# Kernel optimization log

Measured on AMD Instinct MI355X. Metric: run time of the kernel, lower is better.

The kernel has to match this reference:

```python
import jax, jax.numpy as jnp
import numpy as np

D_MODEL, D_QKV, N_HEADS = 1024, 64, 16


def setup_inputs() -> dict:
    key = jax.random.key(0)
    k_x, k_qkv, k_out = jax.random.split(key, 3)
    X = jax.random.normal(k_x, (2, 2048, D_MODEL), dtype=jnp.float32)
    # nn.Linear(d_model, 3*d_qkv*n_heads, bias=False): store as (in, out) for X @ W
    W_qkv = jax.random.normal(k_qkv, (D_MODEL, 3 * D_QKV * N_HEADS), dtype=jnp.float32) * (D_MODEL ** -0.5)
    W_out = jax.random.normal(k_out, (D_QKV * N_HEADS, D_MODEL), dtype=jnp.float32) * ((D_QKV * N_HEADS) ** -0.5)
    return {"X": X, "W_qkv": W_qkv, "W_out": W_out}


def reference(X, W_qkv, W_out):
    b, s, _ = X.shape
    h, d = N_HEADS, D_QKV
    scale = d ** 0.5
    qkv = X @ W_qkv                          # [b, s, 3*h*d]
    # Faithful to torch: view(b, s, h, d, 3).unbind(-1) -> interleaved q/k/v layout
    qkv = qkv.reshape(b, s, h, d, 3)
    q, k, v = qkv[..., 0], qkv[..., 1], qkv[..., 2]   # each [b, s, h, d]
    scores = jnp.einsum("bqhd,bkhd->bhqk", q, k) / scale
    weights = jax.nn.softmax(scores, axis=-1)          # [b, h, s, s]
    attn = jnp.einsum("bhqk,bkhd->bqhd", weights, v)   # [b, s, h, d]
    return attn.reshape(b, s, h * d) @ W_out           # [b, s, d_model]
```

## Files before the change

### kernel.cpp

```cpp
#include <hip/hip_runtime.h>
#include <hip/hip_bf16.h>
#include <math.h>

typedef __bf16 bf16;
typedef __bf16 bf16x2 __attribute__((ext_vector_type(2)));
typedef __bf16 bf16x4 __attribute__((ext_vector_type(4)));
typedef __bf16 bf16x8 __attribute__((ext_vector_type(8)));
typedef float f32x2 __attribute__((ext_vector_type(2)));
typedef float f32x4 __attribute__((ext_vector_type(4)));
typedef float f32x16 __attribute__((ext_vector_type(16)));
typedef int i32x2 __attribute__((ext_vector_type(2)));
typedef int i32x4 __attribute__((ext_vector_type(4)));

#define MFMA16(a, b, c) __builtin_amdgcn_mfma_f32_16x16x32_bf16(a, b, c, 0, 0, 0)
#define MFMA32(a, b, c) __builtin_amdgcn_mfma_f32_32x32x16_bf16(a, b, c, 0, 0, 0)

constexpr int D_MODEL = 1024;
constexpr int N_QKV   = 3072;
constexpr int BATCH   = 2;
constexpr int SEQ     = 2048;
constexpr int NH      = 16;
constexpr int DH      = 64;
constexpr int M_TOT   = BATCH * SEQ;

__device__ __forceinline__ void gl_lds16(const bf16* g, bf16* l) {
    __builtin_amdgcn_global_load_lds(
        (const __attribute__((address_space(1))) void*)g,
        (__attribute__((address_space(3))) void*)l, 16, 0, 0);
}

__device__ __forceinline__ void pl32swap(int& a, int& b) {
    i32x2 r = __builtin_amdgcn_permlane32_swap(a, b, false, false);
    a = r[0];
    b = r[1];
}

template <int N> __device__ __forceinline__ void waitv() {
    asm volatile("s_waitcnt vmcnt(%0)" :: "n"(N) : "memory");
}
__device__ __forceinline__ void waitlgkm0() {
    asm volatile("s_waitcnt lgkmcnt(0)" ::: "memory");
}

__device__ __forceinline__ void transpose_tile(
    const float* __restrict__ in, bf16* __restrict__ out,
    int K, int N, int n0, int k0, bf16 (*T)[72], bool permute)
{
    const int tid = threadIdx.x;
    const int r   = tid >> 2;
    const int c4  = (tid & 3) * 16;

    const float* src = in + (size_t)(k0 + r) * N + n0 + c4;
    f32x4 v0 = *(const f32x4*)(src + 0);
    f32x4 v1 = *(const f32x4*)(src + 4);
    f32x4 v2 = *(const f32x4*)(src + 8);
    f32x4 v3 = *(const f32x4*)(src + 12);
    #pragma unroll
    for (int j = 0; j < 4; j++) {
        T[c4 + j][r]      = (bf16)v0[j];
        T[c4 + 4 + j][r]  = (bf16)v1[j];
        T[c4 + 8 + j][r]  = (bf16)v2[j];
        T[c4 + 12 + j][r] = (bf16)v3[j];
    }
    __syncthreads();
    int rowg = n0 + r;
    if (permute) {
        const int which = rowg % 3;
        const int h     = rowg / 192;
        const int d     = (rowg % 192) / 3;
        rowg = which * 1024 + h * 64 + d;
    }
    bf16* dst = out + (size_t)rowg * K + k0 + c4;
    *(bf16x8*)(dst)     = *(const bf16x8*)&T[r][c4];
    *(bf16x8*)(dst + 8) = *(const bf16x8*)&T[r][c4 + 8];
}

__global__ __launch_bounds__(256) void prepass_kernel(
    const float* __restrict__ X, const float* __restrict__ Wqkv,
    const float* __restrict__ Wout,
    bf16* __restrict__ xb, bf16* __restrict__ wqkv_t, bf16* __restrict__ wout_t)
{
    __shared__ bf16 T[64][72];
    const int b = blockIdx.x;
    if (b < 2048) {
        const size_t i = ((size_t)b * 256 + threadIdx.x) * 8;
        f32x4 a0 = *(const f32x4*)(X + i);
        f32x4 a1 = *(const f32x4*)(X + i + 4);
        bf16x8 w;
        #pragma unroll
        for (int j = 0; j < 4; j++) { w[j] = (bf16)a0[j]; w[j + 4] = (bf16)a1[j]; }
        *(bf16x8*)(xb + i) = w;
    } else if (b < 2048 + 768) {
        const int idx = b - 2048;
        transpose_tile(Wqkv, wqkv_t, D_MODEL, N_QKV,
                       (idx % 48) * 64, (idx / 48) * 64, T, true);
    } else {
        const int idx = b - 2816;
        transpose_tile(Wout, wout_t, D_MODEL, D_MODEL,
                       (idx % 16) * 64, (idx / 16) * 64, T, false);
    }
}

__global__ __launch_bounds__(512, 2) void qkv_gemm_kernel(
    const bf16* __restrict__ Xb, const bf16* __restrict__ Wt,
    bf16* __restrict__ qb, bf16* __restrict__ kb, bf16* __restrict__ vb)
{
    __shared__ __align__(16) bf16 smem[65536];
    bf16* const sA = smem;
    bf16* const sB = smem + 32768;

    const int tid  = threadIdx.x;
    const int wave = tid >> 6;
    const int lane = tid & 63;
    const int quad = lane >> 4;
    const int l16  = lane & 15;
    const int wr   = wave >> 2;
    const int wc   = wave & 3;
    const int m0   = blockIdx.x * 256;
    const int n0   = blockIdx.y * 256;

    const int sr2  = tid >> 3;
    const int c8p  = (tid & 7) ^ (sr2 & 7);
    const int stR0 = (sr2 << 1) | (c8p >> 2);
    const int stC0 = (c8p & 3) << 3;

    const bf16* Asrc = Xb + (size_t)(m0 + stR0) * D_MODEL + stC0;
    const bf16* Bsrc = Wt + (size_t)(n0 + stR0) * D_MODEL + stC0;

#define STG(s, kbo)                                                          \
    do {                                                                     \
        gl_lds16(Asrc + (kbo),                 sA + (s) * 8192 + tid * 8);   \
        gl_lds16(Asrc + 128 * D_MODEL + (kbo), sA + (s) * 8192 + 4096 + tid * 8); \
        gl_lds16(Bsrc + (kbo),                 sB + (s) * 8192 + tid * 8);   \
        gl_lds16(Bsrc + 128 * D_MODEL + (kbo), sB + (s) * 8192 + 4096 + tid * 8); \
    } while (0)

    const int foff = ((l16 >> 1) << 6) +
                     (((((l16 & 1) << 2) | quad) ^ ((l16 >> 1) & 7)) << 3);

    f32x4 acc[8][4];
    #pragma unroll
    for (int a = 0; a < 8; a++)
        #pragma unroll
        for (int b = 0; b < 4; b++) acc[a][b] = {0.f, 0.f, 0.f, 0.f};

    bf16x8 afA[8], bfA[4], afB[8], bfB[4];

    STG(0, 0); STG(1, 32); STG(2, 64);
    waitv<4>();
    __builtin_amdgcn_s_barrier();
    {
        const bf16* A0 = sA + wr * 4096;
        const bf16* B0 = sB + wc * 2048;
        #pragma unroll
        for (int mi = 0; mi < 8; mi++)
            afA[mi] = *(const bf16x8*)&A0[mi * 512 + foff];
        #pragma unroll
        for (int ni = 0; ni < 4; ni++)
            bfA[ni] = *(const bf16x8*)&B0[ni * 512 + foff];
    }

    int p = 0;

#define PHASE(CA, CB, NA, NB, DOSTG, DONXT, WV)                              \
    {                                                                        \
        if (DOSTG) { const int kst = p + 3; STG((kst & 3), kst * 32); }      \
        const int sn = (p + 1) & 3;                                          \
        const bf16* An_ = sA + sn * 8192 + wr * 4096;                        \
        const bf16* Bn_ = sB + sn * 8192 + wc * 2048;                        \
        __builtin_amdgcn_s_setprio(1);                                       \
        _Pragma("unroll") for (int c = 0; c < 4; c++) {                      \
            _Pragma("unroll") for (int m2 = 0; m2 < 2; m2++)                 \
                _Pragma("unroll") for (int ni = 0; ni < 4; ni++)             \
                    acc[c * 2 + m2][ni] =                                    \
                        MFMA16(CA[c * 2 + m2], CB[ni], acc[c * 2 + m2][ni]); \
            if (DONXT) {                                                     \
                NA[c * 2]     = *(const bf16x8*)&An_[(c * 2) * 512 + foff];  \
                NA[c * 2 + 1] = *(const bf16x8*)&An_[(c * 2 + 1) * 512 + foff]; \
            }                                                                \
        }                                                                    \
        if (DONXT) {                                                         \
            _Pragma("unroll") for (int ni = 0; ni < 4; ni++)                 \
                NB[ni] = *(const bf16x8*)&Bn_[ni * 512 + foff];              \
        }                                                                    \
        __builtin_amdgcn_s_setprio(0);                                       \
        waitv<WV>();                                                         \
        __builtin_amdgcn_s_barrier();                                        \
        ++p;                                                                 \
    }

    for (int t = 0; t < 14; ++t) {
        PHASE(afA, bfA, afB, bfB, true, true, 4)
        PHASE(afB, bfB, afA, bfA, true, true, 4)
    }
    PHASE(afA, bfA, afB, bfB, true,  true,  4)
    PHASE(afB, bfB, afA, bfA, false, true,  0)
    PHASE(afA, bfA, afB, bfB, false, true,  0)
    PHASE(afB, bfB, afA, bfA, false, false, 0)

#undef PHASE
#undef STG

    const int bb     = m0 >> 11;
    const int s_base = m0 & (SEQ - 1);

    if (n0 < 2048) {
        bf16* dst0 = (n0 < 1024) ? qb : kb;
        const int h = ((n0 + wc * 64) >> 6) & 15;
        const size_t bh = (size_t)(bb * NH + h);
        #pragma unroll
        for (int mi = 0; mi < 8; mi++) {
            const int s0 = s_base + wr * 128 + mi * 16 + quad * 4;
            #pragma unroll
            for (int ni = 0; ni < 4; ni++) {
                const int d = ni * 16 + l16;
                #pragma unroll
                for (int i = 0; i < 4; i++)
                    dst0[(bh * SEQ + s0 + i) * DH + d] = (bf16)acc[mi][ni][i];
            }
        }
    } else {
        __syncthreads();
        bf16* T = smem;
        #pragma unroll
        for (int ni = 0; ni < 4; ni++) {
            const int nl = wc * 64 + ni * 16 + l16;
            #pragma unroll
            for (int mi = 0; mi < 8; mi++) {
                const int ml = wr * 128 + mi * 16 + quad * 4;
                bf16x4 pv;
                #pragma unroll
                for (int i = 0; i < 4; i++) pv[i] = (bf16)acc[mi][ni][i];
                const int c   = ml >> 3;
                const int swz = (c & 24) | ((c ^ nl) & 7);
                *(bf16x4*)&T[nl * 256 + swz * 8 + (ml & 7)] = pv;
            }
        }
        __syncthreads();
        const int hbase = (n0 - 2048) >> 6;
        #pragma unroll
        for (int it = 0; it < 8; it++) {
            const int nl = (tid >> 4) + it * 32;
            const int h  = hbase + (nl >> 6);
            const int d  = nl & 63;
            const size_t obase = ((size_t)(bb * NH + h) * DH + d) * SEQ + s_base;
            #pragma unroll
            for (int cc = 0; cc < 2; cc++) {
                const int c   = (tid & 15) + cc * 16;
                const int swz = (c & 24) | ((c ^ nl) & 7);
                bf16x8 vv = *(const bf16x8*)&T[nl * 256 + swz * 8];
                *(bf16x8*)(vb + obase + c * 8) = vv;
            }
        }
    }
}

__global__ __launch_bounds__(512, 4) void attn_kernel(
    const bf16* __restrict__ qb, const bf16* __restrict__ kb,
    const bf16* __restrict__ vb, bf16* __restrict__ ob)
{
    __shared__ __align__(16) bf16 smem[32768];

    const int tid  = threadIdx.x;
    const int wave = tid >> 6;
    const int grp  = wave >> 2;
    const int wq   = wave & 3;
    const int lane = tid & 63;
    const int l32  = lane & 31;
    const int hi   = lane >> 5;
    const int ltid = tid & 255;
    const int bh   = blockIdx.x;
    const int q0   = blockIdx.y * 128;
    const size_t base  = (size_t)bh * SEQ * DH;
    const int    kbase = grp * (SEQ / 2);

    bf16* const KsB = smem + grp * 2 * 4096;
    bf16* const VtB = smem + 16384 + grp * 2 * 4096;

    constexpr float QSCALE = 0.125f * 1.44269504f;

    bf16x8 qf[4];
    {
        const size_t qoff = base + (size_t)(q0 + wq * 32 + l32) * DH + hi * 8;
        #pragma unroll
        for (int kc = 0; kc < 4; kc++) {
            qf[kc] = *(const bf16x8*)(qb + qoff + kc * 16);
            #pragma unroll
            for (int j = 0; j < 8; j++)
                qf[kc][j] = (bf16)((float)qf[kc][j] * QSCALE);
        }
    }

    f32x16 o_acc[2];
    #pragma unroll
    for (int i = 0; i < 16; i++) { o_acc[0][i] = 0.f; o_acc[1][i] = 0.f; }
    float l_acc = 0.f;

    const int swz = (l32 & 7) ^ (l32 >> 3);

    const int so0 = ltid;
    const int so1 = 256 + ltid;
    const int sr0 = so0 >> 3, sc0 = ((so0 & 7) ^ (sr0 & 7) ^ ((sr0 >> 3) & 3)) * 8;
    const int sr1 = so1 >> 3, sc1 = ((so1 & 7) ^ (sr1 & 7) ^ ((sr1 >> 3) & 3)) * 8;

    #define STAGE(bufi, kk0)                                                   \
        do {                                                                   \
            gl_lds16(kb + base + (size_t)(kbase + (kk0) + sr0) * DH + sc0,     \
                     KsB + (bufi) * 4096 + so0 * 8);                           \
            gl_lds16(kb + base + (size_t)(kbase + (kk0) + sr1) * DH + sc1,     \
                     KsB + (bufi) * 4096 + so1 * 8);                           \
            gl_lds16(vb + base + (size_t)sr0 * SEQ + kbase + (kk0) + sc0,      \
                     VtB + (bufi) * 4096 + so0 * 8);                           \
            gl_lds16(vb + base + (size_t)sr1 * SEQ + kbase + (kk0) + sc1,      \
                     VtB + (bufi) * 4096 + so1 * 8);                           \
        } while (0)

    STAGE(0, 0);
    int buf = 0;

    for (int kt = 0; kt < SEQ / 128; ++kt) {
        __syncthreads();
        if (kt + 1 < SEQ / 128) STAGE(buf ^ 1, (kt + 1) * 64);

        const bf16* Kst = KsB + buf * 4096;
        const bf16* Vtt = VtB + buf * 4096;

        #pragma unroll
        for (int kblk = 0; kblk < 2; kblk++) {
            f32x16 sacc;
            #pragma unroll
            for (int i = 0; i < 16; i++) sacc[i] = 0.f;
            #pragma unroll
            for (int kc = 0; kc < 4; kc++) {
                const int cko = ((2 * kc + hi) ^ swz) * 8;
                bf16x8 kf = *(const bf16x8*)
                    &Kst[(kblk * 32 + l32) * 64 + cko];
                sacc = MFMA32(kf, qf[kc], sacc);
            }

            int w[8];
            #pragma unroll
            for (int c = 0; c < 8; c++) {
                const float e0 = __builtin_amdgcn_exp2f(sacc[2 * c]);
                const float e1 = __builtin_amdgcn_exp2f(sacc[2 * c + 1]);
                l_acc += e0;
                l_acc += e1;
                bf16x2 t; t[0] = (bf16)e0; t[1] = (bf16)e1;
                w[c] = __builtin_bit_cast(int, t);
            }
            #pragma unroll
            for (int cc = 0; cc < 2; cc++) {
                pl32swap(w[cc * 4 + 0], w[cc * 4 + 2]);
                pl32swap(w[cc * 4 + 1], w[cc * 4 + 3]);
                i32x4 fi = {w[cc * 4 + 0], w[cc * 4 + 1],
                            w[cc * 4 + 2], w[cc * 4 + 3]};
                bf16x8 pa = __builtin_bit_cast(bf16x8, fi);

                const int kc = kblk * 2 + cc;
                const int cko = ((2 * kc + hi) ^ swz) * 8;
                #pragma unroll
                for (int nb = 0; nb < 2; nb++) {
                    bf16x8 vf = *(const bf16x8*)
                        &Vtt[(nb * 32 + l32) * 64 + cko];
                    o_acc[nb] = MFMA32(pa, vf, o_acc[nb]);
                }
            }
        }
        buf ^= 1;
    }
    #undef STAGE

    const float l_q = l_acc + __shfl_xor(l_acc, 32);

    float* cO  = (float*)smem;
    float* cL1 = (float*)smem + 8192;
    float* cL2 = (float*)smem + 8320;

    __syncthreads();
    if (grp == 1) {
        #pragma unroll
        for (int nb = 0; nb < 2; nb++)
            #pragma unroll
            for (int c4 = 0; c4 < 4; c4++) {
                const int j = nb * 4 + c4;
                f32x4 v = { o_acc[nb][c4 * 4 + 0], o_acc[nb][c4 * 4 + 1],
                            o_acc[nb][c4 * 4 + 2], o_acc[nb][c4 * 4 + 3] };
                *(f32x4*)&cO[(wq * 64 + lane) * 32 + ((j ^ (lane & 7)) * 4)] = v;
            }
        if (hi == 0) cL1[wq * 32 + l32] = l_q;
    }
    __syncthreads();
    if (grp == 0) {
        #pragma unroll
        for (int nb = 0; nb < 2; nb++)
            #pragma unroll
            for (int c4 = 0; c4 < 4; c4++) {
                const int j = nb * 4 + c4;
                f32x4 v = *(const f32x4*)
                    &cO[(wq * 64 + lane) * 32 + ((j ^ (lane & 7)) * 4)];
                #pragma unroll
                for (int e = 0; e < 4; e++) o_acc[nb][c4 * 4 + e] += v[e];
            }
        if (hi == 0) cL2[wq * 32 + l32] = l_q + cL1[wq * 32 + l32];
    }
    __syncthreads();
    if (grp == 0) {
        const int b = bh >> 4, h = bh & 15;
        #pragma unroll
        for (int i = 0; i < 16; i++) {
            const int qrow = (i & 3) + 8 * (i >> 2) + 4 * hi;
            const int q = q0 + wq * 32 + qrow;
            const float li = 1.0f / cL2[wq * 32 + qrow];
            #pragma unroll
            for (int nb = 0; nb < 2; nb++)
                ob[((size_t)(b * SEQ + q) * NH + h) * DH + nb * 32 + l32] =
                    (bf16)(o_acc[nb][i] * li);
        }
    }
}

__global__ __launch_bounds__(256, 2) void out_gemm_kernel(
    const bf16* __restrict__ A, const bf16* __restrict__ Wt,
    float* __restrict__ out)
{
    __shared__ __align__(16) bf16 smem[32768];
    bf16* const sA = smem;
    bf16* const sB = smem + 16384;

    const int tid  = threadIdx.x;
    const int wave = tid >> 6;
    const int lane = tid & 63;
    const int quad = lane >> 4;
    const int l16  = lane & 15;
    const int wr   = wave >> 1;
    const int wc   = wave & 1;
    const int m0   = blockIdx.x * 128;
    const int n0   = blockIdx.y * 128;

    const int sr2  = tid >> 3;
    const int c8p  = (tid & 7) ^ (sr2 & 7);
    const int stR0 = (sr2 << 1) | (c8p >> 2);
    const int stC0 = (c8p & 3) << 3;

    const bf16* Asrc = A  + (size_t)(m0 + stR0) * D_MODEL + stC0;
    const bf16* Bsrc = Wt + (size_t)(n0 + stR0) * D_MODEL + stC0;

#define STG(s, kbo)                                                          \
    do {                                                                     \
        gl_lds16(Asrc + (kbo),                sA + (s) * 4096 + tid * 8);    \
        gl_lds16(Asrc + 64 * D_MODEL + (kbo), sA + (s) * 4096 + 2048 + tid * 8); \
        gl_lds16(Bsrc + (kbo),                sB + (s) * 4096 + tid * 8);    \
        gl_lds16(Bsrc + 64 * D_MODEL + (kbo), sB + (s) * 4096 + 2048 + tid * 8); \
    } while (0)

    const int foff = ((l16 >> 1) << 6) +
                     (((((l16 & 1) << 2) | quad) ^ ((l16 >> 1) & 7)) << 3);

    f32x4 acc[4][4];
    #pragma unroll
    for (int a = 0; a < 4; a++)
        #pragma unroll
        for (int b = 0; b < 4; b++) acc[a][b] = {0.f, 0.f, 0.f, 0.f};

#define PHASE(s, jn, DOSTG, WV)                                              \
    {                                                                        \
        const bf16* Ab_ = sA + (s) * 4096 + wr * 2048;                       \
        const bf16* Bb_ = sB + (s) * 4096 + wc * 2048;                       \
        bf16x8 af[4], bfr[4];                                                \
        _Pragma("unroll") for (int mi = 0; mi < 4; mi++)                     \
            af[mi] = *(const bf16x8*)&Ab_[mi * 512 + foff];                  \
        _Pragma("unroll") for (int ni = 0; ni < 4; ni++)                     \
            bfr[ni] = *(const bf16x8*)&Bb_[ni * 512 + foff];                 \
        waitlgkm0();                                                         \
        __builtin_amdgcn_s_barrier();                                        \
        if (DOSTG) { STG((s), (jn) * 32); }                                  \
        __builtin_amdgcn_s_setprio(1);                                       \
        _Pragma("unroll") for (int mi = 0; mi < 4; mi++)                     \
            _Pragma("unroll") for (int ni = 0; ni < 4; ni++)                 \
                acc[mi][ni] = MFMA16(af[mi], bfr[ni], acc[mi][ni]);          \
        __builtin_amdgcn_s_setprio(0);                                       \
        waitv<WV>();                                                         \
        __builtin_amdgcn_s_barrier();                                        \
    }

    STG(0, 0); STG(1, 32); STG(2, 64); STG(3, 96);
    waitv<12>();
    __builtin_amdgcn_s_barrier();

    for (int t = 0; t < 7; ++t) {
        const int j = t * 4;
        PHASE(0, j + 4, true, 12)
        PHASE(1, j + 5, true, 12)
        PHASE(2, j + 6, true, 12)
        PHASE(3, j + 7, true, 12)
    }
    PHASE(0, 0, false, 8)
    PHASE(1, 0, false, 4)
    PHASE(2, 0, false, 0)
    PHASE(3, 0, false, 0)

#undef PHASE
#undef STG

    #pragma unroll
    for (int mi = 0; mi < 4; mi++) {
        const int row0 = m0 + wr * 64 + mi * 16 + quad * 4;
        #pragma unroll
        for (int ni = 0; ni < 4; ni++) {
            const int n = n0 + wc * 64 + ni * 16 + l16;
            #pragma unroll
            for (int i = 0; i < 4; i++)
                out[(size_t)(row0 + i) * D_MODEL + n] = acc[mi][ni][i];
        }
    }
}

extern "C" void kernel_launch(void* const* d_in, const int* in_sizes, int n_in,
                              void* d_out, int out_size, void* d_ws, size_t ws_size,
                              hipStream_t stream)
{
    const float* X    = (const float*)d_in[0];
    const float* Wqkv = (const float*)d_in[1];
    const float* Wout = (const float*)d_in[2];
    float* out        = (float*)d_out;

    const size_t n_elem = (size_t)M_TOT * D_MODEL;
    bf16* qb      = (bf16*)d_ws;
    bf16* kb      = qb + n_elem;
    bf16* vb      = kb + n_elem;
    bf16* attnb   = vb + n_elem;
    bf16* wqkv_t  = attnb + n_elem;
    bf16* wout_t  = wqkv_t + (size_t)N_QKV * D_MODEL;
    bf16* xb      = wout_t + (size_t)D_MODEL * D_MODEL;

    prepass_kernel<<<3072, 256, 0, stream>>>(X, Wqkv, Wout, xb, wqkv_t, wout_t);

    qkv_gemm_kernel<<<dim3(M_TOT / 256, N_QKV / 256), 512, 0, stream>>>(
        xb, wqkv_t, qb, kb, vb);
    attn_kernel<<<dim3(BATCH * NH, SEQ / 128), 512, 0, stream>>>(qb, kb, vb, attnb);
    out_gemm_kernel<<<dim3(M_TOT / 128, D_MODEL / 128), 256, 0, stream>>>(
        attnb, wout_t, out);
}
```

Measured before the change: 166.7 us.

## Double-buffer LDS fragment reads in output GEMM, overlapping them with MFMAs

Restructures the output-projection GEMM main loop so that the LDS fragment loads for the next k-stage are issued while the current stage's MFMAs run, using two register fragment sets (A/B ping-pong). Prefetch depth drops from four stages to three, and one barrier per phase is removed. This is meant to hide LDS read latency and barrier stalls behind the matrix instructions, at the cost of more registers and a shallower global prefetch.

```diff
diff --git a/kernel.cpp b/kernel.cpp
--- a/kernel.cpp
+++ b/kernel.cpp
@@ -37,9 +37,6 @@
 
 template <int N> __device__ __forceinline__ void waitv() {
     asm volatile("s_waitcnt vmcnt(%0)" :: "n"(N) : "memory");
-}
-__device__ __forceinline__ void waitlgkm0() {
-    asm volatile("s_waitcnt lgkmcnt(0)" ::: "memory");
 }
 
 __device__ __forceinline__ void transpose_tile(
@@ -462,42 +459,54 @@
         #pragma unroll
         for (int b = 0; b < 4; b++) acc[a][b] = {0.f, 0.f, 0.f, 0.f};
 
-#define PHASE(s, jn, DOSTG, WV)                                              \
+    bf16x8 afA[4], bfA[4], afB[4], bfB[4];
+
+    STG(0, 0); STG(1, 32); STG(2, 64);
+    waitv<4>();
+    __builtin_amdgcn_s_barrier();
+    {
+        const bf16* A0 = sA + wr * 2048;
+        const bf16* B0 = sB + wc * 2048;
+        #pragma unroll
+        for (int mi = 0; mi < 4; mi++)
+            afA[mi] = *(const bf16x8*)&A0[mi * 512 + foff];
+        #pragma unroll
+        for (int ni = 0; ni < 4; ni++)
+            bfA[ni] = *(const bf16x8*)&B0[ni * 512 + foff];
+    }
+
+    int p = 0;
+
+#define PHASE(CA, CB, NA, NB, DOSTG, DONXT, WV)                              \
     {                                                                        \
-        const bf16* Ab_ = sA + (s) * 4096 + wr * 2048;                       \
-        const bf16* Bb_ = sB + (s) * 4096 + wc * 2048;                       \
-        bf16x8 af[4], bfr[4];                                                \
-        _Pragma("unroll") for (int mi = 0; mi < 4; mi++)                     \
-            af[mi] = *(const bf16x8*)&Ab_[mi * 512 + foff];                  \
-        _Pragma("unroll") for (int ni = 0; ni < 4; ni++)                     \
-            bfr[ni] = *(const bf16x8*)&Bb_[ni * 512 + foff];                 \
-        waitlgkm0();                                                         \
-        __builtin_amdgcn_s_barrier();                                        \
-        if (DOSTG) { STG((s), (jn) * 32); }                                  \
+        if (DOSTG) { const int kst = p + 3; STG((kst & 3), kst * 32); }      \
+        const int sn = (p + 1) & 3;                                          \
+        const bf16* An_ = sA + sn * 4096 + wr * 2048;                        \
+        const bf16* Bn_ = sB + sn * 4096 + wc * 2048;                        \
         __builtin_amdgcn_s_setprio(1);                                       \
-        _Pragma("unroll") for (int mi = 0; mi < 4; mi++)                     \
+        _Pragma("unroll") for (int mi = 0; mi < 4; mi++) {                   \
             _Pragma("unroll") for (int ni = 0; ni < 4; ni++)                 \
-                acc[mi][ni] = MFMA16(af[mi], bfr[ni], acc[mi][ni]);          \
+                acc[mi][ni] = MFMA16(CA[mi], CB[ni], acc[mi][ni]);           \
+            if (DONXT) NA[mi] = *(const bf16x8*)&An_[mi * 512 + foff];       \
+        }                                                                    \
+        if (DONXT) {                                                         \
+            _Pragma("unroll") for (int ni = 0; ni < 4; ni++)                 \
+                NB[ni] = *(const bf16x8*)&Bn_[ni * 512 + foff];              \
+        }                                                                    \
         __builtin_amdgcn_s_setprio(0);                                       \
         waitv<WV>();                                                         \
         __builtin_amdgcn_s_barrier();                                        \
-    }
-
-    STG(0, 0); STG(1, 32); STG(2, 64); STG(3, 96);
-    waitv<12>();
-    __builtin_amdgcn_s_barrier();
-
-    for (int t = 0; t < 7; ++t) {
-        const int j = t * 4;
-        PHASE(0, j + 4, true, 12)
-        PHASE(1, j + 5, true, 12)
-        PHASE(2, j + 6, true, 12)
-        PHASE(3, j + 7, true, 12)
-    }
-    PHASE(0, 0, false, 8)
-    PHASE(1, 0, false, 4)
-    PHASE(2, 0, false, 0)
-    PHASE(3, 0, false, 0)
+        ++p;                                                                 \
+    }
+
+    for (int t = 0; t < 14; ++t) {
+        PHASE(afA, bfA, afB, bfB, true, true, 4)
+        PHASE(afB, bfB, afA, bfA, true, true, 4)
+    }
+    PHASE(afA, bfA, afB, bfB, true,  true,  4)
+    PHASE(afB, bfB, afA, bfA, false, true,  0)
+    PHASE(afA, bfA, afB, bfB, false, true,  0)
+    PHASE(afB, bfB, afA, bfA, false, false, 0)
 
 #undef PHASE
 #undef STG
```

Measured after the change: 160.4 us. -3.8%, faster.
